# Optimization experiments

Hardware: AMD Instinct MI355X
Metric: run time of the kernel (lower is better)

## Reference

```python
import jax, jax.numpy as jnp
import numpy as np

B, S, D = 2, 2048, 4096
H, HD = 32, 128  # n_heads, head_dim
P = 30           # prefix_len
ROPE_THETA = 10000.0


def _rope_tables():
    inv = 1.0 / (ROPE_THETA ** (np.arange(0, HD, 2, dtype=np.float64) / HD))
    f = np.outer(np.arange(S, dtype=np.float64), inv)  # [S, HD/2]
    return jnp.asarray(np.cos(f), jnp.float32), jnp.asarray(np.sin(f), jnp.float32)


def setup_inputs() -> dict:
    key = jax.random.key(0)
    ks = jax.random.split(key, 7)
    scale = 0.02
    x = jax.random.normal(ks[0], (B, S, D), jnp.float32)
    freqs_cos, freqs_sin = _rope_tables()
    prefix = jax.random.normal(ks[1], (1, P, D), jnp.float32) * scale
    prefix_gate = jax.random.normal(ks[2], (H,), jnp.float32) * 0.1
    wq = jax.random.normal(ks[3], (D, H * HD), jnp.float32) * scale
    wk = jax.random.normal(ks[4], (D, H * HD), jnp.float32) * scale
    wv = jax.random.normal(ks[5], (D, H * HD), jnp.float32) * scale
    wo = jax.random.normal(ks[6], (H * HD, D), jnp.float32) * scale
    return dict(x=x, freqs_cos=freqs_cos, freqs_sin=freqs_sin, prefix=prefix,
                prefix_gate=prefix_gate, wq=wq, wk=wk, wv=wv, wo=wo, start_pos=0)


def _apply_rope(t, cos, sin):
    # t: [b, s, h, hd]; cos/sin: [s, hd/2] -> broadcast [1, s, 1, hd/2]
    tr = t.reshape(*t.shape[:-1], HD // 2, 2)
    t0, t1 = tr[..., 0], tr[..., 1]
    c = cos[None, :, None, :]
    s = sin[None, :, None, :]
    o0 = t0 * c - t1 * s
    o1 = t0 * s + t1 * c
    return jnp.stack([o0, o1], axis=-1).reshape(t.shape)


def _attend(q, k, v, causal):
    # q: [b, sq, h, d]; k, v: [b, sk, h, d]
    scale = 1.0 / jnp.sqrt(jnp.asarray(HD, q.dtype))
    scores = jnp.einsum('bqhd,bkhd->bhqk', q, k) * scale
    if causal:
        sq, sk = q.shape[1], k.shape[1]
        mask = jnp.tril(jnp.ones((sq, sk), bool))
        scores = jnp.where(mask[None, None], scores, jnp.asarray(-1e30, scores.dtype))
    probs = jax.nn.softmax(scores, axis=-1)
    return jnp.einsum('bhqk,bkhd->bqhd', probs, v)


def reference(x, freqs_cos, freqs_sin, prefix, prefix_gate, wq, wk, wv, wo, start_pos):
    bsz, seqlen, _ = x.shape
    xq = (x @ wq).reshape(bsz, seqlen, H, HD)
    xk = (x @ wk).reshape(bsz, seqlen, H, HD)
    xv = (x @ wv).reshape(bsz, seqlen, H, HD)
    xq = _apply_rope(xq, freqs_cos, freqs_sin)
    xk = _apply_rope(xk, freqs_cos, freqs_sin)
    # n_rep == 1 (MHA), repeat_kv is identity
    out = _attend(xq, xk, xv, causal=True)  # [b, s, h, hd]
    # prefix-tuning branch: no RoPE on prefix k/v, non-causal attention
    pk = jnp.broadcast_to(prefix @ wk, (bsz, P, H * HD)).reshape(bsz, P, H, HD)
    pv = jnp.broadcast_to(prefix @ wv, (bsz, P, H * HD)).reshape(bsz, P, H, HD)
    prefix_delta = _attend(xq, pk, pv, causal=False)
    gate = jnp.tanh(prefix_gate).reshape(1, 1, H, 1)
    out = out + gate * prefix_delta
    out = out.reshape(bsz, seqlen, H * HD)
    return out @ wo
```

## Files before the change

kernel.cpp:

```cpp
#include <hip/hip_runtime.h>
#include <hip/hip_bf16.h>

#define AS1 __attribute__((address_space(1)))
#define AS3 __attribute__((address_space(3)))

typedef __attribute__((ext_vector_type(8))) short bf16x8;
typedef __attribute__((ext_vector_type(4))) float f32x4;

#define B_ 2
#define S_ 2048
#define D_ 4096
#define H_ 32
#define HD_ 128
#define P_ 30

__device__ __forceinline__ short f2b(float f) {
  union { __hip_bfloat16 h; short s; } u;
  u.h = __float2bfloat16(f);
  return u.s;
}
__device__ __forceinline__ float b2f(short s) {
  union { short s; __hip_bfloat16 h; } u;
  u.s = s;
  return __bfloat162float(u.h);
}
__device__ __forceinline__ void gload16(const void* g, void* l) {
  __builtin_amdgcn_global_load_lds((const AS1 void*)g, (AS3 void*)l, 16, 0, 0);
}

__global__ __launch_bounds__(256) void convert_f32_bf16(const float* __restrict__ in,
                                                        short* __restrict__ out) {
  size_t i = ((size_t)blockIdx.x * 256 + threadIdx.x) * 4;
  float4 v = *reinterpret_cast<const float4*>(in + i);
  short4 o;
  o.x = f2b(v.x); o.y = f2b(v.y); o.z = f2b(v.z); o.w = f2b(v.w);
  *reinterpret_cast<short4*>(out + i) = o;
}

__global__ __launch_bounds__(256) void pad_prefix(const float* __restrict__ p,
                                                  short* __restrict__ pb) {
  int i = blockIdx.x * 256 + threadIdx.x;
  int row = i >> 12, col = i & 4095;
  pb[i] = (row < P_) ? f2b(p[row * D_ + col]) : (short)0;
}

__global__ void transpose_convert(const float* __restrict__ W, short* __restrict__ Wt,
                                  int K, int N) {
  __shared__ float t[32][33];
  int bx = blockIdx.x, by = blockIdx.y;
  int tx = threadIdx.x, ty = threadIdx.y;
#pragma unroll
  for (int i = 0; i < 4; ++i) {
    int r = ty * 4 + i;
    t[r][tx] = W[(size_t)(by * 32 + r) * N + bx * 32 + tx];
  }
  __syncthreads();
#pragma unroll
  for (int i = 0; i < 4; ++i) {
    int r = ty * 4 + i;
    Wt[(size_t)(bx * 32 + r) * K + by * 32 + tx] = f2b(t[tx][r]);
  }
}

__global__ __launch_bounds__(256) void rope_kernel(short* __restrict__ q,
                                                   short* __restrict__ k,
                                                   const float* __restrict__ fc,
                                                   const float* __restrict__ fs) {
  short* t = blockIdx.y ? k : q;
  const float qs = blockIdx.y ? 1.0f : 0.08838834764831845f;
  size_t g = ((size_t)blockIdx.x * 256 + threadIdx.x) * 8;
  int d = (int)(g & 127);
  int s = (int)((g >> 12) & 2047);
  bf16x8 v = *reinterpret_cast<bf16x8*>(t + g);
  int i0 = d >> 1;
  float4 c = *reinterpret_cast<const float4*>(fc + (size_t)s * 64 + i0);
  float4 sn = *reinterpret_cast<const float4*>(fs + (size_t)s * 64 + i0);
  float cc[4] = {c.x, c.y, c.z, c.w};
  float ss[4] = {sn.x, sn.y, sn.z, sn.w};
  bf16x8 o;
#pragma unroll
  for (int p = 0; p < 4; ++p) {
    float t0 = b2f(v[2 * p]), t1 = b2f(v[2 * p + 1]);
    o[2 * p] = f2b((t0 * cc[p] - t1 * ss[p]) * qs);
    o[2 * p + 1] = f2b((t0 * ss[p] + t1 * cc[p]) * qs);
  }
  *reinterpret_cast<bf16x8*>(t + g) = o;
}

template <int OM>
__global__ __launch_bounds__(256) void gemm_bt(const short* __restrict__ A,
                                               const short* __restrict__ Bt,
                                               void* __restrict__ Cv,
                                               int M, int N, int K) {
  __shared__ short As[128 * 32];
  __shared__ short Bs[128 * 32];
  const int tid = threadIdx.x;
  const int lane = tid & 63;
  const int wbase = tid & 192;
  const int wr = ((tid >> 7) & 1) * 64;
  const int wc = ((tid >> 6) & 1) * 64;
  const int lr = lane & 15;
  const int lk = (lane >> 4) * 8;
  int lin = blockIdx.y * gridDim.x + blockIdx.x;
  int nwg = gridDim.x * gridDim.y;
  int cpx = nwg >> 3;
  int swz = (lin & 7) * cpx + (lin >> 3);
  const int bm = swz / gridDim.x, bn = swz % gridDim.x;
  f32x4 acc[4][4] = {};
  const short* Ab = A + (size_t)bm * 128 * K;
  const short* Bb = Bt + (size_t)bn * 128 * K;
  for (int kt = 0; kt < K; kt += 32) {
    __syncthreads();
#pragma unroll
    for (int i = 0; i < 2; ++i) {
      int f = i * 256 + tid;
      int row = f >> 2, col = (f & 3) * 8;
      gload16(Ab + (size_t)row * K + kt + col, &As[(i * 256 + wbase) * 8]);
      gload16(Bb + (size_t)row * K + kt + col, &Bs[(i * 256 + wbase) * 8]);
    }
    __syncthreads();
    bf16x8 af[4], bfr[4];
#pragma unroll
    for (int m = 0; m < 4; ++m)
      af[m] = *reinterpret_cast<const bf16x8*>(&As[(wr + m * 16 + lr) * 32 + lk]);
#pragma unroll
    for (int n = 0; n < 4; ++n)
      bfr[n] = *reinterpret_cast<const bf16x8*>(&Bs[(wc + n * 16 + lr) * 32 + lk]);
#pragma unroll
    for (int m = 0; m < 4; ++m)
#pragma unroll
      for (int n = 0; n < 4; ++n)
        acc[m][n] = __builtin_amdgcn_mfma_f32_16x16x32_bf16(af[m], bfr[n], acc[m][n], 0, 0, 0);
  }
  const int row0 = bm * 128 + wr + (lane >> 4) * 4;
  const int col0 = bn * 128 + wc + lr;
  if constexpr (OM == 3) {
    short* C = (short*)Cv;
#pragma unroll
    for (int m = 0; m < 4; ++m)
#pragma unroll
      for (int n = 0; n < 4; ++n) {
        short4 pk;
        pk.x = f2b(acc[m][n][0]); pk.y = f2b(acc[m][n][1]);
        pk.z = f2b(acc[m][n][2]); pk.w = f2b(acc[m][n][3]);
        size_t idx = (size_t)(col0 + n * 16) * M + row0 + m * 16;
        *reinterpret_cast<short4*>(&C[idx]) = pk;
      }
  } else {
#pragma unroll
    for (int m = 0; m < 4; ++m)
#pragma unroll
      for (int n = 0; n < 4; ++n)
#pragma unroll
        for (int j = 0; j < 4; ++j) {
          size_t idx = (size_t)(row0 + m * 16 + j) * N + col0 + n * 16;
          ((short*)Cv)[idx] = f2b(acc[m][n][j]);
        }
  }
}

#define MFMA16(mh)                                                              \
  _Pragma("unroll") for (int mm = 0; mm < 4; ++mm)                              \
    _Pragma("unroll") for (int nn = 0; nn < 4; ++nn)                            \
      acc[(mh)*4 + mm][nn] = __builtin_amdgcn_mfma_f32_16x16x32_bf16(           \
          af[mm], bf[nn], acc[(mh)*4 + mm][nn], 0, 0, 0);

template <int OM>
__global__ __launch_bounds__(512, 2) void gemm256(const short* __restrict__ A,
                                                  const short* __restrict__ Bt,
                                                  void* __restrict__ Cv,
                                                  int M, int N, int K) {
  __shared__ short As[2][256 * 64];
  __shared__ short Bs[2][256 * 64];
  const int tid = threadIdx.x;
  const int w = tid >> 6;
  const int lane = tid & 63;
  const int lr = lane & 15, lg = lane >> 4;
  const int wr = (w >> 2) * 128;
  const int wc = (w & 3) * 64;
  int lin = blockIdx.y * gridDim.x + blockIdx.x;
  int nwg = gridDim.x * gridDim.y;
  int cpx = nwg >> 3;
  int swz = (lin & 7) * cpx + (lin >> 3);
  const int bm = swz / gridDim.x, bn = swz % gridDim.x;

  const short* Ab = A + (size_t)bm * 256 * K;
  const short* Bb = Bt + (size_t)bn * 256 * K;
  const int NT = K >> 6;

  f32x4 acc[8][4] = {};

  auto stA = [&](int slot_, int r0, int kt) {
    int row = r0 + (lane >> 3);
    int gsrc = (lane & 7) ^ ((lane >> 3) & 7);
    gload16(Ab + (size_t)row * K + kt + gsrc * 8, &As[slot_][r0 * 64]);
  };
  auto stB = [&](int slot_, int r0, int kt) {
    int row = r0 + (lane >> 3);
    int gsrc = (lane & 7) ^ ((lane >> 3) & 7);
    gload16(Bb + (size_t)row * K + kt + gsrc * 8, &Bs[slot_][r0 * 64]);
  };

  const int q2 = w * 2, q4 = w * 4;
  const int rt0 = (q2 < 8 ? 0 : 64) + q2 * 8;
  const int rt1 = (q2 + 1 < 8 ? 0 : 64) + (q2 + 1) * 8;

  auto stageTile = [&](int slot_, int kt) {
#pragma unroll
    for (int i = 0; i < 4; ++i) stB(slot_, (q4 + i) * 8, kt);
    stA(slot_, rt0, kt); stA(slot_, 64 + rt0, kt);
    stA(slot_, rt1, kt); stA(slot_, 64 + rt1, kt);
  };

  stageTile(0, 0);
  asm volatile("s_waitcnt vmcnt(0)" ::: "memory");
  __builtin_amdgcn_s_barrier();

  for (int t = 0; t < NT; ++t) {
    const int slot = t & 1;
    const int ns = slot ^ 1;
    if (t + 1 < NT) stageTile(ns, (t + 1) << 6);

#pragma unroll
    for (int kh = 0; kh < 2; ++kh) {
      const int pg = ((kh * 4 + lg) ^ (lr & 7)) * 8;
      bf16x8 bf[4], af[4];
#pragma unroll
      for (int nn = 0; nn < 4; ++nn)
        bf[nn] = *(const bf16x8*)&Bs[slot][(wc + nn * 16 + lr) * 64 + pg];
#pragma unroll
      for (int mm = 0; mm < 4; ++mm)
        af[mm] = *(const bf16x8*)&As[slot][(wr + mm * 16 + lr) * 64 + pg];
      __builtin_amdgcn_s_setprio(1);
      MFMA16(0)
      __builtin_amdgcn_s_setprio(0);
#pragma unroll
      for (int mm = 0; mm < 4; ++mm)
        af[mm] = *(const bf16x8*)&As[slot][(wr + 64 + mm * 16 + lr) * 64 + pg];
      __builtin_amdgcn_s_setprio(1);
      MFMA16(1)
      __builtin_amdgcn_s_setprio(0);
    }

    asm volatile("s_waitcnt vmcnt(0)" ::: "memory");
    __builtin_amdgcn_s_barrier();
  }

  const int row0 = bm * 256 + wr + lg * 4;
  const int col0 = bn * 256 + wc + lr;
  if constexpr (OM == 2) {
    short* C = (short*)Cv;
#pragma unroll
    for (int mf = 0; mf < 8; ++mf)
#pragma unroll
      for (int n = 0; n < 4; ++n) {
        int r0 = row0 + mf * 16;
        int bb = r0 >> 11, s0 = r0 & 2047;
        short4 pk;
        pk.x = f2b(acc[mf][n][0]); pk.y = f2b(acc[mf][n][1]);
        pk.z = f2b(acc[mf][n][2]); pk.w = f2b(acc[mf][n][3]);
        size_t idx = ((size_t)(bb * 4096 + col0 + n * 16)) * 2048 + s0;
        *reinterpret_cast<short4*>(&C[idx]) = pk;
      }
  } else {
#pragma unroll
    for (int mf = 0; mf < 8; ++mf)
#pragma unroll
      for (int n = 0; n < 4; ++n)
#pragma unroll
        for (int j = 0; j < 4; ++j) {
          size_t idx = (size_t)(row0 + mf * 16 + j) * N + col0 + n * 16;
          if constexpr (OM == 1) ((short*)Cv)[idx] = f2b(acc[mf][n][j]);
          else ((float*)Cv)[idx] = acc[mf][n][j];
        }
  }
}

__global__ __launch_bounds__(1024, 4) void attn_kernel(
    const short* __restrict__ qb, const short* __restrict__ kb, const short* __restrict__ vt,
    const short* __restrict__ pkb, const short* __restrict__ pvt,
    const float* __restrict__ gate, short* __restrict__ ab) {
  __shared__ short Ks[2][64 * 128];
  __shared__ short Vs[2][128 * 64];
  __shared__ short Ps[16][16 * 64];
  const int tid = threadIdx.x;
  const int wave = tid >> 6, lane = tid & 63;
  const int lr = lane & 15, lg = lane >> 4;
  const int lin = blockIdx.x;
  const int qt = 7 - (lin >> 6);
  const int bh = lin & 63;
  const int b = bh >> 5, h = bh & 31;

  bf16x8 aq[4];
  {
    const short* qrow = qb + ((size_t)(b * S_ + qt * 256 + wave * 16 + lr) * H_ + h) * HD_;
#pragma unroll
    for (int kk = 0; kk < 4; ++kk)
      aq[kk] = *reinterpret_cast<const bf16x8*>(qrow + kk * 32 + lg * 8);
  }

  float m = -1e30f, l = 0.f, l2 = 0.f;
  f32x4 o[8] = {}, o2[8] = {};

  const short* kb_bh = kb + ((size_t)b * S_ * H_ + h) * HD_;
  const short* vt_bh = vt + ((size_t)(b * H_ + h)) * HD_ * S_;

  auto stageK = [&](int t, int buf) {
    int row = tid >> 4;
    int col = ((tid & 15) ^ (row & 7)) * 8;
    gload16(kb_bh + (size_t)(t * 64 + row) * (H_ * HD_) + col,
            &Ks[buf][(tid & 960) * 8]);
  };
  auto stagePK = [&](int buf) {
    int row = tid >> 4;
    int col = ((tid & 15) ^ (row & 7)) * 8;
    gload16(pkb + (size_t)row * 4096 + h * HD_ + col, &Ks[buf][(tid & 960) * 8]);
  };
  auto stageV = [&](int t, int buf) {
    int row = tid >> 3;
    int col = ((tid & 7) ^ (row & 7)) * 8;
    gload16(vt_bh + (size_t)row * S_ + t * 64 + col, &Vs[buf][(tid & 1016) * 8]);
  };
  auto stagePV = [&](int buf) {
    int row = tid >> 3;
    int col = ((tid & 7) ^ (row & 7)) * 8;
    gload16(pvt + ((size_t)h * HD_ + row) * 128 + col, &Vs[buf][(tid & 1016) * 8]);
  };

  auto qkt = [&](int buf, f32x4 sc[4]) {
    __builtin_amdgcn_s_setprio(1);
#pragma unroll
    for (int cb = 0; cb < 4; ++cb) {
      int tok = cb * 16 + lr;
#pragma unroll
      for (int kk = 0; kk < 4; ++kk) {
        int addr = tok * 128 + (((kk * 4 + lg) ^ (tok & 7)) * 8);
        bf16x8 bk = *reinterpret_cast<const bf16x8*>(&Ks[buf][addr]);
        sc[cb] = __builtin_amdgcn_mfma_f32_16x16x32_bf16(bk, aq[kk], sc[cb], 0, 0, 0);
      }
    }
    __builtin_amdgcn_s_setprio(0);
  };
  auto pv = [&](int buf, f32x4* acc_) {
#pragma unroll
    for (int kk = 0; kk < 2; ++kk) {
      bf16x8 ap = *reinterpret_cast<const bf16x8*>(
          &Ps[wave][lr * 64 + (((kk * 4 + lg) ^ (lr & 7)) * 8)]);
      __builtin_amdgcn_s_setprio(1);
#pragma unroll
      for (int nb = 0; nb < 8; ++nb) {
        int d = nb * 16 + lr;
        bf16x8 bv = *reinterpret_cast<const bf16x8*>(
            &Vs[buf][d * 64 + (((kk * 4 + lg) ^ (lr & 7)) * 8)]);
        acc_[nb] = __builtin_amdgcn_mfma_f32_16x16x32_bf16(ap, bv, acc_[nb], 0, 0, 0);
      }
      __builtin_amdgcn_s_setprio(0);
    }
  };

  auto process = [&](int t, bool diag) {
    const int buf = t & 1;
    f32x4 sc[4] = {};
    qkt(buf, sc);
    if (diag) {
      const int rowg = qt * 256 + wave * 16 + lr;
#pragma unroll
      for (int cb = 0; cb < 4; ++cb)
#pragma unroll
        for (int j = 0; j < 4; ++j) {
          int colg = t * 64 + cb * 16 + lg * 4 + j;
          if (colg > rowg) sc[cb][j] = -1e30f;
        }
    }
    float mx = sc[0][0];
#pragma unroll
    for (int cb = 0; cb < 4; ++cb)
#pragma unroll
      for (int j = 0; j < 4; ++j) mx = fmaxf(mx, sc[cb][j]);
    mx = fmaxf(mx, __shfl_xor(mx, 16));
    mx = fmaxf(mx, __shfl_xor(mx, 32));
    if (!__all(mx <= m + 8.f)) {
      float mn = fmaxf(m, mx);
      float alpha = __expf(m - mn);
      m = mn;
      l *= alpha;
      f32x4 av;
#pragma unroll
      for (int j = 0; j < 4; ++j) av[j] = __shfl(alpha, lg * 4 + j);
#pragma unroll
      for (int nb = 0; nb < 8; ++nb)
#pragma unroll
        for (int j = 0; j < 4; ++j) o[nb][j] *= av[j];
    }
    float rs = 0.f;
#pragma unroll
    for (int cb = 0; cb < 4; ++cb) {
      short4 pk;
      float p0 = __expf(sc[cb][0] - m);
      float p1 = __expf(sc[cb][1] - m);
      float p2 = __expf(sc[cb][2] - m);
      float p3 = __expf(sc[cb][3] - m);
      rs += (p0 + p1) + (p2 + p3);
      pk.x = f2b(p0); pk.y = f2b(p1); pk.z = f2b(p2); pk.w = f2b(p3);
      int gran = (cb * 2 + (lg >> 1)) ^ (lr & 7);
      *reinterpret_cast<short4*>(&Ps[wave][lr * 64 + gran * 8 + (lg & 1) * 4]) = pk;
    }
    rs += __shfl_xor(rs, 16);
    rs += __shfl_xor(rs, 32);
    l += rs;
    pv(buf, o);
  };

  auto processPrefix = [&]() {
    f32x4 sc[4] = {};
    qkt(0, sc);
#pragma unroll
    for (int cb = 0; cb < 4; ++cb)
#pragma unroll
      for (int j = 0; j < 4; ++j) {
        int coll = cb * 16 + lg * 4 + j;
        if (coll >= P_) sc[cb][j] = -1e30f;
      }
    float mx = sc[0][0];
#pragma unroll
    for (int cb = 0; cb < 4; ++cb)
#pragma unroll
      for (int j = 0; j < 4; ++j) mx = fmaxf(mx, sc[cb][j]);
    mx = fmaxf(mx, __shfl_xor(mx, 16));
    mx = fmaxf(mx, __shfl_xor(mx, 32));
    float rs = 0.f;
#pragma unroll
    for (int cb = 0; cb < 4; ++cb) {
      short4 pk;
      float p0 = __expf(sc[cb][0] - mx);
      float p1 = __expf(sc[cb][1] - mx);
      float p2 = __expf(sc[cb][2] - mx);
      float p3 = __expf(sc[cb][3] - mx);
      rs += (p0 + p1) + (p2 + p3);
      pk.x = f2b(p0); pk.y = f2b(p1); pk.z = f2b(p2); pk.w = f2b(p3);
      int gran = (cb * 2 + (lg >> 1)) ^ (lr & 7);
      *reinterpret_cast<short4*>(&Ps[wave][lr * 64 + gran * 8 + (lg & 1) * 4]) = pk;
    }
    rs += __shfl_xor(rs, 16);
    rs += __shfl_xor(rs, 32);
    l2 = rs;
    pv(0, o2);
  };

  const int nt = 4 * (qt + 1);

  stagePK(0);
  stagePV(0);
  __syncthreads();
  processPrefix();
  __syncthreads();

  stageK(0, 0);
  stageV(0, 0);
  __syncthreads();
  for (int t = 0; t < nt; ++t) {
    if (t + 1 < nt) {
      stageK(t + 1, (t + 1) & 1);
      stageV(t + 1, (t + 1) & 1);
    }
    process(t, t >= 4 * qt);
    __syncthreads();
  }

  {
    float g = tanhf(gate[h]);
    f32x4 lv, lv2;
#pragma unroll
    for (int j = 0; j < 4; ++j) {
      lv[j] = __shfl(l, lg * 4 + j);
      lv2[j] = __shfl(l2, lg * 4 + j);
    }
#pragma unroll
    for (int j = 0; j < 4; ++j) {
      int q = qt * 256 + wave * 16 + lg * 4 + j;
      float inv = 1.f / lv[j];
      float inv2 = g / lv2[j];
      size_t base = ((size_t)(b * S_ + q) * H_ + h) * HD_;
#pragma unroll
      for (int nb = 0; nb < 8; ++nb)
        ab[base + nb * 16 + lr] = f2b(o[nb][j] * inv + o2[nb][j] * inv2);
    }
  }
}

extern "C" void kernel_launch(void* const* d_in, const int* in_sizes, int n_in,
                              void* d_out, int out_size, void* d_ws, size_t ws_size,
                              hipStream_t stream) {
  const float* x = (const float*)d_in[0];
  const float* fc = (const float*)d_in[1];
  const float* fs = (const float*)d_in[2];
  const float* prefix = (const float*)d_in[3];
  const float* gate = (const float*)d_in[4];
  const float* wq = (const float*)d_in[5];
  const float* wk = (const float*)d_in[6];
  const float* wv = (const float*)d_in[7];
  const float* wo = (const float*)d_in[8];
  float* out = (float*)d_out;

  char* ws = (char*)d_ws;
  const size_t SZ = (size_t)4096 * 4096 * 2;
  short* xb = (short*)(ws);
  short* wT = (short*)(ws + SZ);
  short* qbuf = (short*)(ws + 2 * SZ);
  short* kbuf = (short*)(ws + 3 * SZ);
  short* vT = (short*)(ws + 4 * SZ);
  short* pb = (short*)(ws + 5 * SZ);
  short* pkb = (short*)(ws + 5 * SZ + (1 << 20));
  short* pvt = (short*)(ws + 5 * SZ + (2 << 20));
  short* abuf = xb;

  dim3 tcg(128, 128), tcb(32, 8);
  dim3 gg(16, 16), gp(32, 1);

  convert_f32_bf16<<<16384, 256, 0, stream>>>(x, xb);
  pad_prefix<<<2048, 256, 0, stream>>>(prefix, pb);

  transpose_convert<<<tcg, tcb, 0, stream>>>(wq, wT, 4096, 4096);
  gemm256<1><<<gg, 512, 0, stream>>>(xb, wT, qbuf, 4096, 4096, 4096);

  transpose_convert<<<tcg, tcb, 0, stream>>>(wk, wT, 4096, 4096);
  gemm256<1><<<gg, 512, 0, stream>>>(xb, wT, kbuf, 4096, 4096, 4096);
  gemm_bt<1><<<gp, 256, 0, stream>>>(pb, wT, pkb, 128, 4096, 4096);

  transpose_convert<<<tcg, tcb, 0, stream>>>(wv, wT, 4096, 4096);
  gemm256<2><<<gg, 512, 0, stream>>>(xb, wT, vT, 4096, 4096, 4096);
  gemm_bt<3><<<gp, 256, 0, stream>>>(pb, wT, pvt, 128, 4096, 4096);

  rope_kernel<<<dim3(8192, 2), 256, 0, stream>>>(qbuf, kbuf, fc, fs);

  attn_kernel<<<512, 1024, 0, stream>>>(qbuf, kbuf, vT, pkb, pvt, gate, abuf);

  transpose_convert<<<tcg, tcb, 0, stream>>>(wo, wT, 4096, 4096);
  gemm256<0><<<gg, 512, 0, stream>>>(abuf, wT, out, 4096, 4096, 4096);
}
```

Baseline: 924.8 us.

## Use 32x32x16 MFMA with phased, interleaved global prefetch in gemm256

Switches the 256x256 GEMM inner loop from 16x16x32 to 32x32x16 bf16 MFMA tiles, which halves the LDS fragment loads per MFMA flop. It also restructures the K loop into four phases that each issue part of the next tiles' global-to-LDS loads, prefetching two tiles ahead with partial vmcnt waits. Barriers and priority changes are added around each phase. This aims to hide memory latency and reduce LDS traffic, at the cost of more barriers and a more fragile schedule in which a slot can be overwritten while still in use.

```diff
diff --git a/kernel.cpp b/kernel.cpp
--- a/kernel.cpp
+++ b/kernel.cpp
@@ -6,6 +6,7 @@
 
 typedef __attribute__((ext_vector_type(8))) short bf16x8;
 typedef __attribute__((ext_vector_type(4))) float f32x4;
+typedef __attribute__((ext_vector_type(16))) float f32x16;
 
 #define B_ 2
 #define S_ 2048
@@ -159,11 +160,38 @@
   }
 }
 
-#define MFMA16(mh)                                                              \
-  _Pragma("unroll") for (int mm = 0; mm < 4; ++mm)                              \
-    _Pragma("unroll") for (int nn = 0; nn < 4; ++nn)                            \
-      acc[(mh)*4 + mm][nn] = __builtin_amdgcn_mfma_f32_16x16x32_bf16(           \
-          af[mm], bf[nn], acc[(mh)*4 + mm][nn], 0, 0, 0);
+#define PH_SYNC_PRE                                                             \
+  __builtin_amdgcn_s_barrier();                                                 \
+  asm volatile("s_waitcnt lgkmcnt(0)" ::: "memory");                            \
+  __builtin_amdgcn_sched_barrier(0);                                            \
+  __builtin_amdgcn_s_setprio(1);
+
+#define PH_SYNC_POST                                                            \
+  __builtin_amdgcn_s_setprio(0);                                                \
+  __builtin_amdgcn_s_barrier();
+
+#define PHASE32(ks, STAGE, TAIL)                                                \
+  {                                                                             \
+    bf16x8 af[4], bfv[2];                                                       \
+    const int gsel = (ks) * 2 + kg;                                             \
+    _Pragma("unroll") for (int mb = 0; mb < 4; ++mb) {                          \
+      int row = wr + mb * 32 + l31;                                             \
+      af[mb] = *(const bf16x8*)&As[slot][row * 64 + ((gsel ^ (row & 7)) * 8)];  \
+    }                                                                           \
+    _Pragma("unroll") for (int nb = 0; nb < 2; ++nb) {                          \
+      int brow = wc + nb * 32 + l31;                                            \
+      bfv[nb] = *(const bf16x8*)&Bs[slot][brow * 64 + ((gsel ^ (brow & 7)) * 8)];\
+    }                                                                           \
+    STAGE;                                                                      \
+    PH_SYNC_PRE                                                                 \
+    _Pragma("unroll") for (int mb = 0; mb < 4; ++mb)                            \
+      _Pragma("unroll") for (int nb = 0; nb < 2; ++nb)                          \
+        acc[mb][nb] = __builtin_amdgcn_mfma_f32_32x32x16_bf16(                  \
+            af[mb], bfv[nb], acc[mb][nb], 0, 0, 0);                             \
+    __builtin_amdgcn_s_setprio(0);                                              \
+    TAIL;                                                                       \
+    __builtin_amdgcn_s_barrier();                                               \
+  }
 
 template <int OM>
 __global__ __launch_bounds__(512, 2) void gemm256(const short* __restrict__ A,
@@ -175,7 +203,8 @@
   const int tid = threadIdx.x;
   const int w = tid >> 6;
   const int lane = tid & 63;
-  const int lr = lane & 15, lg = lane >> 4;
+  const int l31 = lane & 31;
+  const int kg = lane >> 5;
   const int wr = (w >> 2) * 128;
   const int wc = (w & 3) * 64;
   int lin = blockIdx.y * gridDim.x + blockIdx.x;
@@ -188,7 +217,7 @@
   const short* Bb = Bt + (size_t)bn * 256 * K;
   const int NT = K >> 6;
 
-  f32x4 acc[8][4] = {};
+  f32x16 acc[4][2] = {};
 
   auto stA = [&](int slot_, int r0, int kt) {
     int row = r0 + (lane >> 3);
@@ -205,74 +234,75 @@
   const int rt0 = (q2 < 8 ? 0 : 64) + q2 * 8;
   const int rt1 = (q2 + 1 < 8 ? 0 : 64) + (q2 + 1) * 8;
 
-  auto stageTile = [&](int slot_, int kt) {
-#pragma unroll
-    for (int i = 0; i < 4; ++i) stB(slot_, (q4 + i) * 8, kt);
-    stA(slot_, rt0, kt); stA(slot_, 64 + rt0, kt);
-    stA(slot_, rt1, kt); stA(slot_, 64 + rt1, kt);
-  };
-
-  stageTile(0, 0);
-  asm volatile("s_waitcnt vmcnt(0)" ::: "memory");
+  {
+#pragma unroll
+    for (int i = 0; i < 4; ++i) stB(0, (q4 + i) * 8, 0);
+    stA(0, rt0, 0); stA(0, 64 + rt0, 0);
+    stA(0, rt1, 0); stA(0, 64 + rt1, 0);
+#pragma unroll
+    for (int i = 0; i < 4; ++i) stB(1, (q4 + i) * 8, 64);
+    stA(1, rt0, 64); stA(1, 64 + rt0, 64);
+    stA(1, rt1, 64); stA(1, 64 + rt1, 64);
+  }
+  asm volatile("s_waitcnt vmcnt(8)" ::: "memory");
   __builtin_amdgcn_s_barrier();
 
   for (int t = 0; t < NT; ++t) {
     const int slot = t & 1;
     const int ns = slot ^ 1;
-    if (t + 1 < NT) stageTile(ns, (t + 1) << 6);
-
-#pragma unroll
-    for (int kh = 0; kh < 2; ++kh) {
-      const int pg = ((kh * 4 + lg) ^ (lr & 7)) * 8;
-      bf16x8 bf[4], af[4];
-#pragma unroll
-      for (int nn = 0; nn < 4; ++nn)
-        bf[nn] = *(const bf16x8*)&Bs[slot][(wc + nn * 16 + lr) * 64 + pg];
-#pragma unroll
-      for (int mm = 0; mm < 4; ++mm)
-        af[mm] = *(const bf16x8*)&As[slot][(wr + mm * 16 + lr) * 64 + pg];
-      __builtin_amdgcn_s_setprio(1);
-      MFMA16(0)
-      __builtin_amdgcn_s_setprio(0);
-#pragma unroll
-      for (int mm = 0; mm < 4; ++mm)
-        af[mm] = *(const bf16x8*)&As[slot][(wr + 64 + mm * 16 + lr) * 64 + pg];
-      __builtin_amdgcn_s_setprio(1);
-      MFMA16(1)
-      __builtin_amdgcn_s_setprio(0);
-    }
-
-    asm volatile("s_waitcnt vmcnt(0)" ::: "memory");
-    __builtin_amdgcn_s_barrier();
-  }
-
-  const int row0 = bm * 256 + wr + lg * 4;
-  const int col0 = bn * 256 + wc + lr;
+    const int kt1 = (t + 1) << 6, kt2 = (t + 2) << 6;
+    const bool s6 = (t >= 1) && (t + 1 < NT);
+    const bool s2 = (t + 2 < NT);
+
+    PHASE32(0,
+            { if (s6) { stB(ns, (q4 + 0) * 8, kt1); stB(ns, (q4 + 1) * 8, kt1);
+                        stA(ns, 64 + rt0, kt1);     stA(ns, 64 + rt1, kt1); } },
+            {});
+    PHASE32(1,
+            { if (s6) { stB(ns, (q4 + 2) * 8, kt1); stB(ns, (q4 + 3) * 8, kt1); } },
+            {});
+    PHASE32(2, {}, {});
+    PHASE32(3,
+            { if (s2) { stA(slot, rt0, kt2); stA(slot, rt1, kt2); } },
+            { if (s2) asm volatile("s_waitcnt vmcnt(2)" ::: "memory");
+              else    asm volatile("s_waitcnt vmcnt(0)" ::: "memory"); });
+  }
+
   if constexpr (OM == 2) {
     short* C = (short*)Cv;
 #pragma unroll
-    for (int mf = 0; mf < 8; ++mf)
-#pragma unroll
-      for (int n = 0; n < 4; ++n) {
-        int r0 = row0 + mf * 16;
-        int bb = r0 >> 11, s0 = r0 & 2047;
-        short4 pk;
-        pk.x = f2b(acc[mf][n][0]); pk.y = f2b(acc[mf][n][1]);
-        pk.z = f2b(acc[mf][n][2]); pk.w = f2b(acc[mf][n][3]);
-        size_t idx = ((size_t)(bb * 4096 + col0 + n * 16)) * 2048 + s0;
-        *reinterpret_cast<short4*>(&C[idx]) = pk;
+    for (int mb = 0; mb < 4; ++mb)
+#pragma unroll
+      for (int nb = 0; nb < 2; ++nb) {
+        int rbase = bm * 256 + wr + mb * 32;
+        int bb = rbase >> 11, s0 = (rbase & 2047) + 4 * kg;
+        int col = bn * 256 + wc + nb * 32 + l31;
+#pragma unroll
+        for (int rg = 0; rg < 4; ++rg) {
+          short4 pk;
+          pk.x = f2b(acc[mb][nb][rg * 4 + 0]);
+          pk.y = f2b(acc[mb][nb][rg * 4 + 1]);
+          pk.z = f2b(acc[mb][nb][rg * 4 + 2]);
+          pk.w = f2b(acc[mb][nb][rg * 4 + 3]);
+          size_t idx = ((size_t)(bb * 4096 + col)) * 2048 + s0 + rg * 8;
+          *reinterpret_cast<short4*>(&C[idx]) = pk;
+        }
       }
   } else {
 #pragma unroll
-    for (int mf = 0; mf < 8; ++mf)
-#pragma unroll
-      for (int n = 0; n < 4; ++n)
-#pragma unroll
-        for (int j = 0; j < 4; ++j) {
-          size_t idx = (size_t)(row0 + mf * 16 + j) * N + col0 + n * 16;
-          if constexpr (OM == 1) ((short*)Cv)[idx] = f2b(acc[mf][n][j]);
-          else ((float*)Cv)[idx] = acc[mf][n][j];
+    for (int mb = 0; mb < 4; ++mb)
+#pragma unroll
+      for (int nb = 0; nb < 2; ++nb) {
+        int rbase = bm * 256 + wr + mb * 32 + 4 * kg;
+        int col = bn * 256 + wc + nb * 32 + l31;
+#pragma unroll
+        for (int rg = 0; rg < 16; ++rg) {
+          int row = rbase + (rg & 3) + 8 * (rg >> 2);
+          size_t idx = (size_t)row * N + col;
+          if constexpr (OM == 1) ((short*)Cv)[idx] = f2b(acc[mb][nb][rg]);
+          else ((float*)Cv)[idx] = acc[mb][nb][rg];
         }
+      }
   }
 }
 
```

Result: no change. 917.6 us (-0.8%).
